# Kernel optimization log

Hardware: AMD Instinct MI355X
Metric: run time of the kernel (lower is better)

## Reference

```python
import jax, jax.numpy as jnp
import numpy as np

CLIP = 5.0  # clip_value from init


def setup_inputs() -> dict:
    key = jax.random.key(0)
    ks = jax.random.split(key, 6)
    B, T, I, H = 128, 1024, 256, 512
    s = 1.0 / np.sqrt(H)
    return {
        "x": jax.random.normal(ks[0], (B, T, I), dtype=jnp.float32),
        "h0": jax.random.normal(ks[1], (1, H), dtype=jnp.float32),
        "w_ih": jax.random.normal(ks[2], (3 * H, I), dtype=jnp.float32) * s,
        "w_hh": jax.random.normal(ks[3], (3 * H, H), dtype=jnp.float32) * s,
        "b_ih": jax.random.normal(ks[4], (3 * H,), dtype=jnp.float32) * s,
        "b_hh": jax.random.normal(ks[5], (3 * H,), dtype=jnp.float32) * s,
    }


def reference(x, h0, w_ih, w_hh, b_ih, b_hh):
    # x: [B, T, I], h0: [1, H]
    B = x.shape[0]
    h_init = jnp.tile(h0, (B, 1))  # [B, H]
    # Precompute all input projections in one big GEMM: [T, B, 3H]
    gi_all = jnp.einsum('bti,gi->tbg', x, w_ih) + b_ih

    def step(h, gi):
        gh = h @ w_hh.T + b_hh                      # [B, 3H]
        ir, iz, inn = jnp.split(gi, 3, axis=-1)
        hr, hz, hn = jnp.split(gh, 3, axis=-1)
        r = jax.nn.sigmoid(ir + hr)
        z = jax.nn.sigmoid(iz + hz)
        n = jnp.tanh(inn + r * hn)
        h_new = (1.0 - z) * n + z * h
        h_new = jnp.clip(h_new, -CLIP, CLIP)
        return h_new, h_new

    h_last, out = jax.lax.scan(step, h_init, gi_all)  # out: [T, B, H]
    output = jnp.transpose(out, (1, 0, 2))            # [B, T, H]
    return output, h_last
```

## Files before the change

kernel.cpp:

```cpp
#include <hip/hip_runtime.h>
#include <math.h>

#define T_SEQ 1024
#define B_SZ  128
#define I_SZ  256
#define H_SZ  512
#define G_SZ  1536

#define NBS   8
#define MB    16
#define NHS   8
#define HB    64
#define GB    192
#define NTHR  384
#define PGB   384
#define PH    (MB * H_SZ)

#define SENT32 0x7FFF7FFFu

typedef _Float16 f16;
typedef _Float16 half8 __attribute__((ext_vector_type(8)));
typedef _Float16 f16x4 __attribute__((ext_vector_type(4)));
typedef float f32x4 __attribute__((ext_vector_type(4)));
typedef unsigned uint32x2 __attribute__((ext_vector_type(2)));
typedef unsigned uint32x4 __attribute__((ext_vector_type(4)));

__device__ __forceinline__ f32x4 cload_f4(const void* p) {
    f32x4 v;
    asm volatile("global_load_dwordx4 %0, %1, off sc0 sc1" : "=v"(v) : "v"(p));
    return v;
}
__device__ __forceinline__ void cstore_u2(void* p, uint32x2 v) {
    asm volatile("global_store_dwordx2 %0, %1, off sc0 sc1" :: "v"(p), "v"(v) : "memory");
}
__device__ __forceinline__ f16x4 load_f16x4_nw(const void* p) {
    f16x4 v;
    asm volatile("global_load_dwordx2 %0, %1, off" : "=v"(v) : "v"(p));
    return v;
}
__device__ __forceinline__ void wait_vm0() {
    asm volatile("s_waitcnt vmcnt(0)" ::: "memory");
    __builtin_amdgcn_sched_barrier(0);
}
__device__ __forceinline__ bool stale4(f32x4 v) {
    uint32x4 u = __builtin_bit_cast(uint32x4, v);
    return (u[0] == SENT32) | (u[1] == SENT32) | (u[2] == SENT32) | (u[3] == SENT32);
}

__global__ void setup_kernel(const float* __restrict__ w_ih,
                             const float* __restrict__ w_hh,
                             const float* __restrict__ h0,
                             f16* __restrict__ wp16,
                             f16* __restrict__ wf16,
                             f16* __restrict__ hbuf) {
    const size_t i0 = (size_t)blockIdx.x * blockDim.x + threadIdx.x;
    const size_t stride = (size_t)gridDim.x * blockDim.x;
    for (size_t i = i0; i < (size_t)I_SZ * G_SZ; i += stride)
        wp16[i] = (f16)w_ih[i];
    for (size_t i = i0; i < (size_t)NHS * GB * H_SZ; i += stride) {
        int hs  = (int)(i / (GB * H_SZ));
        int rem = (int)(i % (GB * H_SZ));
        int gl = rem / H_SZ, k = rem % H_SZ;
        int gate = gl >> 6, c = gl & 63;
        int gg = gate * H_SZ + hs * HB + c;
        wf16[i] = (f16)w_hh[(size_t)gg * H_SZ + k];
    }
    for (size_t i = i0; i < (size_t)NBS * PH; i += stride)
        hbuf[i] = (f16)h0[i & (H_SZ - 1)];
    const uint32x4 sv = {SENT32, SENT32, SENT32, SENT32};
    const size_t base = (size_t)NBS * PH;
    const size_t nv   = (size_t)T_SEQ * NBS * PH / 8;
    for (size_t i = i0; i < nv; i += stride)
        *reinterpret_cast<uint32x4*>(hbuf + base + i * 8) = sv;
}

__global__ __launch_bounds__(512, 1)
void proj_kernel(const float* __restrict__ x,
                 const f16* __restrict__ wp16,
                 const float* __restrict__ b_ih,
                 f16* __restrict__ gi16) {
    const int t  = blockIdx.x >> 2;
    const int g0 = (blockIdx.x & 3) * PGB;
    const int tid  = threadIdx.x;
    const int wid  = tid >> 6;
    const int lane = tid & 63;
    const int col  = lane & 15;
    const int krow = lane >> 4;

    __shared__ __align__(16) unsigned char x_lds[128 * 512];

    #pragma unroll
    for (int j = 0; j < 8; ++j) {
        int idx = tid + j * 512;
        int b = idx >> 5, k16 = idx & 31;
        const float* xp = x + ((size_t)b * T_SEQ + t) * I_SZ + k16 * 8;
        float4 v0 = *reinterpret_cast<const float4*>(xp);
        float4 v1 = *reinterpret_cast<const float4*>(xp + 4);
        half8 hv;
        hv[0] = (f16)v0.x; hv[1] = (f16)v0.y; hv[2] = (f16)v0.z; hv[3] = (f16)v0.w;
        hv[4] = (f16)v1.x; hv[5] = (f16)v1.y; hv[6] = (f16)v1.z; hv[7] = (f16)v1.w;
        unsigned addr = ((unsigned)(b * 512 + k16 * 16)) ^ (((unsigned)(b & 7)) << 4);
        *reinterpret_cast<half8*>(x_lds + addr) = hv;
    }

    const int gw0 = g0 + wid * 48;
    half8 af[3][8];
    #pragma unroll
    for (int m = 0; m < 3; ++m)
        #pragma unroll
        for (int k = 0; k < 8; ++k)
            af[m][k] = *reinterpret_cast<const half8*>(
                wp16 + (size_t)(gw0 + m * 16 + col) * I_SZ + k * 32 + krow * 8);

    float bias[3][4];
    #pragma unroll
    for (int m = 0; m < 3; ++m)
        #pragma unroll
        for (int r = 0; r < 4; ++r)
            bias[m][r] = b_ih[gw0 + m * 16 + krow * 4 + r];

    __syncthreads();

    #pragma unroll
    for (int nt = 0; nt < 8; ++nt) {
        const int b0 = nt * 16;
        f32x4 acc0 = {0.f,0.f,0.f,0.f}, acc1 = {0.f,0.f,0.f,0.f}, acc2 = {0.f,0.f,0.f,0.f};
        const int brow = b0 + col;
        const unsigned bswz = ((unsigned)(brow & 7)) << 4;
        #pragma unroll
        for (int k = 0; k < 8; ++k) {
            half8 bf = *reinterpret_cast<const half8*>(
                x_lds + (((unsigned)(brow * 512 + k * 64 + krow * 16)) ^ bswz));
            acc0 = __builtin_amdgcn_mfma_f32_16x16x32_f16(af[0][k], bf, acc0, 0, 0, 0);
            acc1 = __builtin_amdgcn_mfma_f32_16x16x32_f16(af[1][k], bf, acc1, 0, 0, 0);
            acc2 = __builtin_amdgcn_mfma_f32_16x16x32_f16(af[2][k], bf, acc2, 0, 0, 0);
        }
        const int pbs = brow >> 4;
        const int pm  = brow & 15;
        #pragma unroll
        for (int r = 0; r < 4; ++r) {
            int gr = gw0 + krow * 4 + r;
            gi16[((size_t)(t * NBS + pbs) * G_SZ + gr)      * MB + pm] = (f16)(acc0[r] + bias[0][r]);
            gi16[((size_t)(t * NBS + pbs) * G_SZ + gr + 16) * MB + pm] = (f16)(acc1[r] + bias[1][r]);
            gi16[((size_t)(t * NBS + pbs) * G_SZ + gr + 32) * MB + pm] = (f16)(acc2[r] + bias[2][r]);
        }
    }
}

__global__ __launch_bounds__(NTHR, 1)
void gru_persist(const f16* __restrict__ gi,
                 const f16* __restrict__ wf16,
                 const float* __restrict__ h0,
                 const float* __restrict__ b_hh,
                 f16* __restrict__ hbuf,
                 float* __restrict__ out) {
    const int bs  = blockIdx.x & (NBS - 1);
    const int hs  = blockIdx.x >> 3;
    const int tid = threadIdx.x;

    __shared__ __align__(16) unsigned char w_lds[96 * 1024];
    __shared__ __align__(16) unsigned char h_lds[MB * H_SZ * 2];
    __shared__ float act_r[MB][HB + 1];
    __shared__ float act_z[MB][HB + 1];
    __shared__ float act_n[MB][HB + 1];
    __shared__ float act_i[MB][HB + 1];

    const int wid  = tid >> 6;
    const int lane = tid & 63;
    const int col  = lane & 15;
    const int krow = lane >> 4;

    const int ttR = wid, ttL = wid + 6;
    const int gateR = ttR >> 2, gateL = ttL >> 2;
    const int gcR = (ttR & 3) * 16 + col;
    const int gcL = (ttL & 3) * 16 + col;
    const int ggR = gateR * H_SZ + hs * HB + gcR;
    const int ggL = gateL * H_SZ + hs * HB + gcL;
    const float biasR = b_hh[ggR];
    const float biasL = b_hh[ggL];

    const f16* wbase = wf16 + (size_t)hs * GB * H_SZ;

    for (int i = tid; i < 96 * 64; i += NTHR) {
        int r = i >> 6, k8 = i & 63;
        f32x4 v = *reinterpret_cast<const f32x4*>(
            wbase + (size_t)(96 + r) * H_SZ + k8 * 8);
        unsigned addr = ((unsigned)(r * 1024 + k8 * 16)) ^ (((unsigned)(r & 7)) << 4);
        *reinterpret_cast<f32x4*>(w_lds + addr) = v;
    }
    half8 bfrag[16];
    {
        const f16* wp = wbase + (size_t)(ttR * 16 + col) * H_SZ + krow * 8;
        #pragma unroll
        for (int kk = 0; kk < 16; ++kk)
            bfrag[kk] = *reinterpret_cast<const half8*>(wp + kk * 32);
    }

    const int cb  = tid >> 4;
    const int cc4 = (tid & 15) * 4;
    f32x4 hm = {0.f, 0.f, 0.f, 0.f};
    if (tid < 256) {
        #pragma unroll
        for (int u = 0; u < 4; ++u) hm[u] = h0[hs * HB + cc4 + u];
    }

    const unsigned a_base = (unsigned)(col * 1024 + krow * 16);
    const unsigned a_swz  = ((unsigned)(col & 7)) << 4;
    const unsigned b_base = (unsigned)((wid * 16 + col) * 1024 + krow * 16);

    const int i0 = tid, i1 = tid + NTHR, i2 = tid + 2 * NTHR;
    const bool has2 = (tid < 256);

    __syncthreads();

    for (int t = 0; t < T_SEQ; ++t) {
        const f16* hin  = hbuf + ((size_t)t       * NBS + bs) * PH;
        f16*       hpub = hbuf + ((size_t)(t + 1) * NBS + bs) * PH;

        f16x4 gvR = load_f16x4_nw(
            gi + ((size_t)(t * NBS + bs) * G_SZ + ggR) * MB + krow * 4);
        f16x4 gvL = load_f16x4_nw(
            gi + ((size_t)(t * NBS + bs) * G_SZ + ggL) * MB + krow * 4);

        __builtin_amdgcn_s_sleep(8);

        const f16* a0p = hin + (i0 >> 6) * H_SZ + (i0 & 63) * 8;
        const f16* a1p = hin + (i1 >> 6) * H_SZ + (i1 & 63) * 8;
        const f16* a2p = hin + (i2 >> 6) * H_SZ + (i2 & 63) * 8;
        f32x4 v0 = cload_f4(a0p);
        f32x4 v1 = cload_f4(a1p);
        f32x4 v2;
        if (has2) v2 = cload_f4(a2p);
        wait_vm0();
        {
            int guard = 0;
            bool s0 = stale4(v0), s1 = stale4(v1), s2 = has2 && stale4(v2);
            while (__any(s0 | s1 | s2)) {
                if (s0) v0 = cload_f4((const void*)a0p);
                if (s1) v1 = cload_f4((const void*)a1p);
                if (s2) v2 = cload_f4((const void*)a2p);
                wait_vm0();
                s0 = stale4(v0); s1 = stale4(v1); s2 = has2 && stale4(v2);
                if (++guard > (1 << 20)) break;
            }
        }

        {
            unsigned l0 = ((unsigned)((i0 >> 6) * 1024 + (i0 & 63) * 16))
                          ^ (((unsigned)((i0 >> 6) & 7)) << 4);
            *reinterpret_cast<f32x4*>(h_lds + l0) = v0;
            unsigned l1 = ((unsigned)((i1 >> 6) * 1024 + (i1 & 63) * 16))
                          ^ (((unsigned)((i1 >> 6) & 7)) << 4);
            *reinterpret_cast<f32x4*>(h_lds + l1) = v1;
            if (has2) {
                unsigned l2 = ((unsigned)((i2 >> 6) * 1024 + (i2 & 63) * 16))
                              ^ (((unsigned)((i2 >> 6) & 7)) << 4);
                *reinterpret_cast<f32x4*>(h_lds + l2) = v2;
            }
        }
        __syncthreads();

        f32x4 accR = {0.f,0.f,0.f,0.f}, accL = {0.f,0.f,0.f,0.f};
        #pragma unroll
        for (int kk = 0; kk < 16; ++kk) {
            half8 av = *reinterpret_cast<const half8*>(
                h_lds + ((a_base + kk * 64) ^ a_swz));
            half8 bv = *reinterpret_cast<const half8*>(
                w_lds + ((b_base + kk * 64) ^ a_swz));
            accR = __builtin_amdgcn_mfma_f32_16x16x32_f16(av, bfrag[kk], accR, 0, 0, 0);
            accL = __builtin_amdgcn_mfma_f32_16x16x32_f16(av, bv,        accL, 0, 0, 0);
        }
        wait_vm0();

        if (gateR == 0) {
            #pragma unroll
            for (int r = 0; r < 4; ++r)
                act_r[krow * 4 + r][gcR] = accR[r] + biasR + (float)gvR[r];
        } else {
            #pragma unroll
            for (int r = 0; r < 4; ++r)
                act_z[krow * 4 + r][gcR] = accR[r] + biasR + (float)gvR[r];
        }
        if (gateL == 1) {
            #pragma unroll
            for (int r = 0; r < 4; ++r)
                act_z[krow * 4 + r][gcL] = accL[r] + biasL + (float)gvL[r];
        } else {
            #pragma unroll
            for (int r = 0; r < 4; ++r) {
                act_n[krow * 4 + r][gcL] = accL[r] + biasL;
                act_i[krow * 4 + r][gcL] = (float)gvL[r];
            }
        }
        __syncthreads();

        if (tid < 256) {
            float h4[4];
            unsigned short us[4];
            #pragma unroll
            for (int u = 0; u < 4; ++u) {
                int c = cc4 + u;
                float r = 1.f / (1.f + __expf(-act_r[cb][c]));
                float z = 1.f / (1.f + __expf(-act_z[cb][c]));
                float a = act_i[cb][c] + r * act_n[cb][c];
                float n = 1.f - 2.f / (__expf(2.f * a) + 1.f);
                float hn = (1.f - z) * n + z * hm[u];
                hn = fminf(fmaxf(hn, -5.f), 5.f);
                hm[u] = hn;
                h4[u] = hn;
                us[u] = __builtin_bit_cast(unsigned short, (f16)hn);
            }
            uint32x2 pk;
            pk[0] = (unsigned)us[0] | ((unsigned)us[1] << 16);
            pk[1] = (unsigned)us[2] | ((unsigned)us[3] << 16);
            const int hg = hs * HB + cc4;
            cstore_u2(hpub + (size_t)cb * H_SZ + hg, pk);

            const int bg = bs * MB + cb;
            *reinterpret_cast<float4*>(
                out + ((size_t)bg * T_SEQ + t) * H_SZ + hg) =
                make_float4(h4[0], h4[1], h4[2], h4[3]);
            if (t == T_SEQ - 1)
                *reinterpret_cast<float4*>(
                    out + (size_t)B_SZ * T_SEQ * H_SZ + (size_t)bg * H_SZ + hg) =
                    make_float4(h4[0], h4[1], h4[2], h4[3]);
        }
    }
}

extern "C" void kernel_launch(void* const* d_in, const int* in_sizes, int n_in,
                              void* d_out, int out_size, void* d_ws, size_t ws_size,
                              hipStream_t stream) {
    const float* x    = (const float*)d_in[0];
    const float* h0   = (const float*)d_in[1];
    const float* w_ih = (const float*)d_in[2];
    const float* w_hh = (const float*)d_in[3];
    const float* b_ih = (const float*)d_in[4];
    const float* b_hh = (const float*)d_in[5];
    float* out = (float*)d_out;

    char* p = (char*)d_ws;
    f16* wp16 = (f16*)p;   p += (size_t)I_SZ * G_SZ * 2;
    f16* wf16 = (f16*)p;   p += (size_t)NHS * GB * H_SZ * 2;
    f16* hbuf = (f16*)p;   p += (size_t)(T_SEQ + 1) * NBS * PH * 2;
    f16* gi   = (f16*)p;

    setup_kernel<<<2048, 256, 0, stream>>>(w_ih, w_hh, h0, wp16, wf16, hbuf);

    proj_kernel<<<T_SEQ * 4, 512, 0, stream>>>(x, wp16, b_ih, gi);

    gru_persist<<<NBS * NHS, NTHR, 0, stream>>>(gi, wf16, h0, b_hh, hbuf, out);
}
```

Measured before the change: 2.998 ms.

## Fuse GRU gate math into MFMA waves, dropping LDS activation staging and a barrier

The persistent GRU kernel now uses 4 waves instead of 6. Each wave computes the r, z and n tiles for the same 16 hidden columns, so the gate nonlinearity runs straight from the MFMA accumulators. This removes the LDS activation arrays and one __syncthreads per timestep, which shortens the serial critical path. In exchange each wave issues three MFMAs per k-step instead of two, holds more weight data in LDS, and publishes h with scattered 16-bit stores and scalar fp32 output stores instead of vectorized ones. The staleness check now tests each 16-bit half against the sentinel.

New measurement: 2.960 ms. About the same (-1.3%).

```diff
diff --git a/kernel.cpp b/kernel.cpp
--- a/kernel.cpp
+++ b/kernel.cpp
@@ -12,17 +12,16 @@
 #define NHS   8
 #define HB    64
 #define GB    192
-#define NTHR  384
+#define GNTHR 256
 #define PGB   384
 #define PH    (MB * H_SZ)
 
-#define SENT32 0x7FFF7FFFu
+#define SENTU16 0x7FFFu
 
 typedef _Float16 f16;
 typedef _Float16 half8 __attribute__((ext_vector_type(8)));
 typedef _Float16 f16x4 __attribute__((ext_vector_type(4)));
 typedef float f32x4 __attribute__((ext_vector_type(4)));
-typedef unsigned uint32x2 __attribute__((ext_vector_type(2)));
 typedef unsigned uint32x4 __attribute__((ext_vector_type(4)));
 
 __device__ __forceinline__ f32x4 cload_f4(const void* p) {
@@ -30,8 +29,8 @@
     asm volatile("global_load_dwordx4 %0, %1, off sc0 sc1" : "=v"(v) : "v"(p));
     return v;
 }
-__device__ __forceinline__ void cstore_u2(void* p, uint32x2 v) {
-    asm volatile("global_store_dwordx2 %0, %1, off sc0 sc1" :: "v"(p), "v"(v) : "memory");
+__device__ __forceinline__ void cstore_u16(void* p, unsigned v) {
+    asm volatile("global_store_short %0, %1, off sc0 sc1" :: "v"(p), "v"(v) : "memory");
 }
 __device__ __forceinline__ f16x4 load_f16x4_nw(const void* p) {
     f16x4 v;
@@ -44,7 +43,13 @@
 }
 __device__ __forceinline__ bool stale4(f32x4 v) {
     uint32x4 u = __builtin_bit_cast(uint32x4, v);
-    return (u[0] == SENT32) | (u[1] == SENT32) | (u[2] == SENT32) | (u[3] == SENT32);
+    bool s = false;
+    #pragma unroll
+    for (int i = 0; i < 4; ++i) {
+        s |= ((u[i] & 0xFFFFu) == SENTU16);
+        s |= ((u[i] >> 16)     == SENTU16);
+    }
+    return s;
 }
 
 __global__ void setup_kernel(const float* __restrict__ w_ih,
@@ -67,7 +72,7 @@
     }
     for (size_t i = i0; i < (size_t)NBS * PH; i += stride)
         hbuf[i] = (f16)h0[i & (H_SZ - 1)];
-    const uint32x4 sv = {SENT32, SENT32, SENT32, SENT32};
+    const uint32x4 sv = {0x7FFF7FFFu, 0x7FFF7FFFu, 0x7FFF7FFFu, 0x7FFF7FFFu};
     const size_t base = (size_t)NBS * PH;
     const size_t nv   = (size_t)T_SEQ * NBS * PH / 8;
     for (size_t i = i0; i < nv; i += stride)
@@ -147,7 +152,7 @@
     }
 }
 
-__global__ __launch_bounds__(NTHR, 1)
+__global__ __launch_bounds__(GNTHR, 1)
 void gru_persist(const f16* __restrict__ gi,
                  const f16* __restrict__ wf16,
                  const float* __restrict__ h0,
@@ -158,58 +163,48 @@
     const int hs  = blockIdx.x >> 3;
     const int tid = threadIdx.x;
 
-    __shared__ __align__(16) unsigned char w_lds[96 * 1024];
+    __shared__ __align__(16) unsigned char w_lds[128 * 1024];
     __shared__ __align__(16) unsigned char h_lds[MB * H_SZ * 2];
-    __shared__ float act_r[MB][HB + 1];
-    __shared__ float act_z[MB][HB + 1];
-    __shared__ float act_n[MB][HB + 1];
-    __shared__ float act_i[MB][HB + 1];
 
     const int wid  = tid >> 6;
     const int lane = tid & 63;
     const int col  = lane & 15;
     const int krow = lane >> 4;
 
-    const int ttR = wid, ttL = wid + 6;
-    const int gateR = ttR >> 2, gateL = ttL >> 2;
-    const int gcR = (ttR & 3) * 16 + col;
-    const int gcL = (ttL & 3) * 16 + col;
-    const int ggR = gateR * H_SZ + hs * HB + gcR;
-    const int ggL = gateL * H_SZ + hs * HB + gcL;
-    const float biasR = b_hh[ggR];
-    const float biasL = b_hh[ggL];
+    const int cg = hs * HB + wid * 16 + col;
+    const float biasR = b_hh[cg];
+    const float biasZ = b_hh[H_SZ + cg];
+    const float biasN = b_hh[2 * H_SZ + cg];
 
     const f16* wbase = wf16 + (size_t)hs * GB * H_SZ;
 
-    for (int i = tid; i < 96 * 64; i += NTHR) {
+    for (int i = tid; i < 128 * 64; i += GNTHR) {
         int r = i >> 6, k8 = i & 63;
         f32x4 v = *reinterpret_cast<const f32x4*>(
-            wbase + (size_t)(96 + r) * H_SZ + k8 * 8);
+            wbase + (size_t)(64 + r) * H_SZ + k8 * 8);
         unsigned addr = ((unsigned)(r * 1024 + k8 * 16)) ^ (((unsigned)(r & 7)) << 4);
         *reinterpret_cast<f32x4*>(w_lds + addr) = v;
     }
     half8 bfrag[16];
     {
-        const f16* wp = wbase + (size_t)(ttR * 16 + col) * H_SZ + krow * 8;
+        const f16* wp = wbase + (size_t)(wid * 16 + col) * H_SZ + krow * 8;
         #pragma unroll
         for (int kk = 0; kk < 16; ++kk)
             bfrag[kk] = *reinterpret_cast<const half8*>(wp + kk * 32);
     }
 
-    const int cb  = tid >> 4;
-    const int cc4 = (tid & 15) * 4;
-    f32x4 hm = {0.f, 0.f, 0.f, 0.f};
-    if (tid < 256) {
-        #pragma unroll
-        for (int u = 0; u < 4; ++u) hm[u] = h0[hs * HB + cc4 + u];
-    }
-
-    const unsigned a_base = (unsigned)(col * 1024 + krow * 16);
-    const unsigned a_swz  = ((unsigned)(col & 7)) << 4;
-    const unsigned b_base = (unsigned)((wid * 16 + col) * 1024 + krow * 16);
-
-    const int i0 = tid, i1 = tid + NTHR, i2 = tid + 2 * NTHR;
-    const bool has2 = (tid < 256);
+    f32x4 hm;
+    {
+        float h0v = h0[cg];
+        hm[0] = h0v; hm[1] = h0v; hm[2] = h0v; hm[3] = h0v;
+    }
+
+    const unsigned a_swz   = ((unsigned)(col & 7)) << 4;
+    const unsigned a_base  = (unsigned)(col * 1024 + krow * 16);
+    const unsigned bz_base = (unsigned)((wid * 16 + col) * 1024 + krow * 16);
+    const unsigned bn_base = (unsigned)((64 + wid * 16 + col) * 1024 + krow * 16);
+
+    const int prow0 = wid, prow1 = wid + 4, prow2 = wid + 8, prow3 = wid + 12;
 
     __syncthreads();
 
@@ -218,112 +213,81 @@
         f16*       hpub = hbuf + ((size_t)(t + 1) * NBS + bs) * PH;
 
         f16x4 gvR = load_f16x4_nw(
-            gi + ((size_t)(t * NBS + bs) * G_SZ + ggR) * MB + krow * 4);
-        f16x4 gvL = load_f16x4_nw(
-            gi + ((size_t)(t * NBS + bs) * G_SZ + ggL) * MB + krow * 4);
+            gi + ((size_t)(t * NBS + bs) * G_SZ + cg) * MB + krow * 4);
+        f16x4 gvZ = load_f16x4_nw(
+            gi + ((size_t)(t * NBS + bs) * G_SZ + H_SZ + cg) * MB + krow * 4);
+        f16x4 gvN = load_f16x4_nw(
+            gi + ((size_t)(t * NBS + bs) * G_SZ + 2 * H_SZ + cg) * MB + krow * 4);
 
         __builtin_amdgcn_s_sleep(8);
 
-        const f16* a0p = hin + (i0 >> 6) * H_SZ + (i0 & 63) * 8;
-        const f16* a1p = hin + (i1 >> 6) * H_SZ + (i1 & 63) * 8;
-        const f16* a2p = hin + (i2 >> 6) * H_SZ + (i2 & 63) * 8;
+        const f16* a0p = hin + prow0 * H_SZ + lane * 8;
+        const f16* a1p = hin + prow1 * H_SZ + lane * 8;
+        const f16* a2p = hin + prow2 * H_SZ + lane * 8;
+        const f16* a3p = hin + prow3 * H_SZ + lane * 8;
         f32x4 v0 = cload_f4(a0p);
         f32x4 v1 = cload_f4(a1p);
-        f32x4 v2;
-        if (has2) v2 = cload_f4(a2p);
+        f32x4 v2 = cload_f4(a2p);
+        f32x4 v3 = cload_f4(a3p);
         wait_vm0();
         {
             int guard = 0;
-            bool s0 = stale4(v0), s1 = stale4(v1), s2 = has2 && stale4(v2);
-            while (__any(s0 | s1 | s2)) {
-                if (s0) v0 = cload_f4((const void*)a0p);
-                if (s1) v1 = cload_f4((const void*)a1p);
-                if (s2) v2 = cload_f4((const void*)a2p);
+            bool s0 = stale4(v0), s1 = stale4(v1), s2 = stale4(v2), s3 = stale4(v3);
+            while (__any(s0 | s1 | s2 | s3)) {
+                if (s0) v0 = cload_f4(a0p);
+                if (s1) v1 = cload_f4(a1p);
+                if (s2) v2 = cload_f4(a2p);
+                if (s3) v3 = cload_f4(a3p);
                 wait_vm0();
-                s0 = stale4(v0); s1 = stale4(v1); s2 = has2 && stale4(v2);
+                s0 = stale4(v0); s1 = stale4(v1); s2 = stale4(v2); s3 = stale4(v3);
                 if (++guard > (1 << 20)) break;
             }
         }
 
         {
-            unsigned l0 = ((unsigned)((i0 >> 6) * 1024 + (i0 & 63) * 16))
-                          ^ (((unsigned)((i0 >> 6) & 7)) << 4);
+            unsigned l0 = ((unsigned)(prow0 * 1024 + lane * 16)) ^ (((unsigned)(prow0 & 7)) << 4);
+            unsigned l1 = ((unsigned)(prow1 * 1024 + lane * 16)) ^ (((unsigned)(prow1 & 7)) << 4);
+            unsigned l2 = ((unsigned)(prow2 * 1024 + lane * 16)) ^ (((unsigned)(prow2 & 7)) << 4);
+            unsigned l3 = ((unsigned)(prow3 * 1024 + lane * 16)) ^ (((unsigned)(prow3 & 7)) << 4);
             *reinterpret_cast<f32x4*>(h_lds + l0) = v0;
-            unsigned l1 = ((unsigned)((i1 >> 6) * 1024 + (i1 & 63) * 16))
-                          ^ (((unsigned)((i1 >> 6) & 7)) << 4);
             *reinterpret_cast<f32x4*>(h_lds + l1) = v1;
-            if (has2) {
-                unsigned l2 = ((unsigned)((i2 >> 6) * 1024 + (i2 & 63) * 16))
-                              ^ (((unsigned)((i2 >> 6) & 7)) << 4);
-                *reinterpret_cast<f32x4*>(h_lds + l2) = v2;
-            }
+            *reinterpret_cast<f32x4*>(h_lds + l2) = v2;
+            *reinterpret_cast<f32x4*>(h_lds + l3) = v3;
         }
         __syncthreads();
 
-        f32x4 accR = {0.f,0.f,0.f,0.f}, accL = {0.f,0.f,0.f,0.f};
+        f32x4 accR = {0.f,0.f,0.f,0.f}, accZ = {0.f,0.f,0.f,0.f}, accN = {0.f,0.f,0.f,0.f};
         #pragma unroll
         for (int kk = 0; kk < 16; ++kk) {
             half8 av = *reinterpret_cast<const half8*>(
                 h_lds + ((a_base + kk * 64) ^ a_swz));
-            half8 bv = *reinterpret_cast<const half8*>(
-                w_lds + ((b_base + kk * 64) ^ a_swz));
+            half8 bz = *reinterpret_cast<const half8*>(
+                w_lds + ((bz_base + kk * 64) ^ a_swz));
+            half8 bn = *reinterpret_cast<const half8*>(
+                w_lds + ((bn_base + kk * 64) ^ a_swz));
             accR = __builtin_amdgcn_mfma_f32_16x16x32_f16(av, bfrag[kk], accR, 0, 0, 0);
-            accL = __builtin_amdgcn_mfma_f32_16x16x32_f16(av, bv,        accL, 0, 0, 0);
-        }
-        wait_vm0();
-
-        if (gateR == 0) {
-            #pragma unroll
-            for (int r = 0; r < 4; ++r)
-                act_r[krow * 4 + r][gcR] = accR[r] + biasR + (float)gvR[r];
-        } else {
-            #pragma unroll
-            for (int r = 0; r < 4; ++r)
-                act_z[krow * 4 + r][gcR] = accR[r] + biasR + (float)gvR[r];
-        }
-        if (gateL == 1) {
-            #pragma unroll
-            for (int r = 0; r < 4; ++r)
-                act_z[krow * 4 + r][gcL] = accL[r] + biasL + (float)gvL[r];
-        } else {
-            #pragma unroll
-            for (int r = 0; r < 4; ++r) {
-                act_n[krow * 4 + r][gcL] = accL[r] + biasL;
-                act_i[krow * 4 + r][gcL] = (float)gvL[r];
-            }
-        }
-        __syncthreads();
-
-        if (tid < 256) {
-            float h4[4];
-            unsigned short us[4];
-            #pragma unroll
-            for (int u = 0; u < 4; ++u) {
-                int c = cc4 + u;
-                float r = 1.f / (1.f + __expf(-act_r[cb][c]));
-                float z = 1.f / (1.f + __expf(-act_z[cb][c]));
-                float a = act_i[cb][c] + r * act_n[cb][c];
-                float n = 1.f - 2.f / (__expf(2.f * a) + 1.f);
-                float hn = (1.f - z) * n + z * hm[u];
-                hn = fminf(fmaxf(hn, -5.f), 5.f);
-                hm[u] = hn;
-                h4[u] = hn;
-                us[u] = __builtin_bit_cast(unsigned short, (f16)hn);
-            }
-            uint32x2 pk;
-            pk[0] = (unsigned)us[0] | ((unsigned)us[1] << 16);
-            pk[1] = (unsigned)us[2] | ((unsigned)us[3] << 16);
-            const int hg = hs * HB + cc4;
-            cstore_u2(hpub + (size_t)cb * H_SZ + hg, pk);
-
-            const int bg = bs * MB + cb;
-            *reinterpret_cast<float4*>(
-                out + ((size_t)bg * T_SEQ + t) * H_SZ + hg) =
-                make_float4(h4[0], h4[1], h4[2], h4[3]);
+            accZ = __builtin_amdgcn_mfma_f32_16x16x32_f16(av, bz,        accZ, 0, 0, 0);
+            accN = __builtin_amdgcn_mfma_f32_16x16x32_f16(av, bn,        accN, 0, 0, 0);
+        }
+
+        #pragma unroll
+        for (int r = 0; r < 4; ++r) {
+            const int b = krow * 4 + r;
+            float rr = 1.f / (1.f + __expf(-(accR[r] + biasR + (float)gvR[r])));
+            float zz = 1.f / (1.f + __expf(-(accZ[r] + biasZ + (float)gvZ[r])));
+            float aa = (float)gvN[r] + rr * (accN[r] + biasN);
+            float nn = 1.f - 2.f / (__expf(2.f * aa) + 1.f);
+            float hn = (1.f - zz) * nn + zz * hm[r];
+            hn = fminf(fmaxf(hn, -5.f), 5.f);
+            hm[r] = hn;
+
+            unsigned us = (unsigned)__builtin_bit_cast(unsigned short, (f16)hn);
+            cstore_u16(hpub + (size_t)b * H_SZ + cg, us);
+
+            const int bg = bs * MB + b;
+            out[((size_t)bg * T_SEQ + t) * H_SZ + cg] = hn;
             if (t == T_SEQ - 1)
-                *reinterpret_cast<float4*>(
-                    out + (size_t)B_SZ * T_SEQ * H_SZ + (size_t)bg * H_SZ + hg) =
-                    make_float4(h4[0], h4[1], h4[2], h4[3]);
+                out[(size_t)B_SZ * T_SEQ * H_SZ + (size_t)bg * H_SZ + cg] = hn;
         }
     }
 }
@@ -349,5 +313,5 @@
 
     proj_kernel<<<T_SEQ * 4, 512, 0, stream>>>(x, wp16, b_ih, gi);
 
-    gru_persist<<<NBS * NHS, NTHR, 0, stream>>>(gi, wf16, h0, b_hh, hbuf, out);
-}
+    gru_persist<<<NBS * NHS, GNTHR, 0, stream>>>(gi, wf16, h0, b_hh, hbuf, out);
+}
```
